# Kernel tuning notes

Measured on AMD Instinct MI355X. Metric: run time of the kernel, lower is better.

## Reference

```python
import jax, jax.numpy as jnp
import numpy as np

D_MODEL = 1024
NUM_HEADS = 16
D_K = D_MODEL // NUM_HEADS
D_FF = 4096


def setup_inputs() -> dict:
    key = jax.random.key(0)
    ks = jax.random.split(key, 12)
    s = 1.0 / np.sqrt(D_MODEL)
    sf = 1.0 / np.sqrt(D_FF)
    return {
        "x": jax.random.normal(ks[0], (2, 2048, D_MODEL), dtype=jnp.float32),
        # nn.Linear weights are [out_features, in_features]
        "Wq": jax.random.uniform(ks[1], (D_MODEL, D_MODEL), jnp.float32, -s, s),
        "Wk": jax.random.uniform(ks[2], (D_MODEL, D_MODEL), jnp.float32, -s, s),
        "Wv": jax.random.uniform(ks[3], (D_MODEL, D_MODEL), jnp.float32, -s, s),
        "Wo": jax.random.uniform(ks[4], (D_MODEL, D_MODEL), jnp.float32, -s, s),
        "W1": jax.random.uniform(ks[5], (D_FF, D_MODEL), jnp.float32, -s, s),
        "W2": jax.random.uniform(ks[6], (D_MODEL, D_FF), jnp.float32, -sf, sf),
        "g1": jnp.ones((D_MODEL,), jnp.float32),
        "b1": jnp.zeros((D_MODEL,), jnp.float32),
        "g2": jnp.ones((D_MODEL,), jnp.float32),
        "b2": jnp.zeros((D_MODEL,), jnp.float32),
    }


def _layer_norm(x, gamma, beta, eps=1e-5):
    mu = jnp.mean(x, axis=-1, keepdims=True)
    var = jnp.mean((x - mu) ** 2, axis=-1, keepdims=True)
    return (x - mu) * jax.lax.rsqrt(var + eps) * gamma + beta


def reference(x, Wq, Wk, Wv, Wo, W1, W2, g1, b1, g2, b2):
    B, S, _ = x.shape
    H, Dk = NUM_HEADS, D_K
    # projections (Linear: x @ W.T), split heads -> [B, H, S, Dk]
    q = (x @ Wq.T).reshape(B, S, H, Dk).transpose(0, 2, 1, 3)
    k = (x @ Wk.T).reshape(B, S, H, Dk).transpose(0, 2, 1, 3)
    v = (x @ Wv.T).reshape(B, S, H, Dk).transpose(0, 2, 1, 3)
    scores = jnp.einsum('bhsd,bhtd->bhst', q, k) / jnp.sqrt(jnp.float32(Dk))
    attn = jax.nn.softmax(scores, axis=-1)
    out = jnp.einsum('bhst,bhtd->bhsd', attn, v)
    out = out.transpose(0, 2, 1, 3).reshape(B, S, H * Dk)
    out = out @ Wo.T
    x_after_attn = _layer_norm(x + out, g1, b1)
    ff = jax.nn.gelu(x_after_attn @ W1.T, approximate=False)
    ff_out = ff @ W2.T
    return _layer_norm(x_after_attn + ff_out, g2, b2)
```

## Files before the change

### kernel.cpp

```cpp
#include <hip/hip_runtime.h>
#include <hip/hip_bf16.h>
#include <cstdint>
#include <cstddef>

#define D_MODEL 1024
#define D_FF    4096
#define NTOK    4096
#define SEQ     2048
#define NH      16
#define DK      64
#define LDQ     3072

typedef __bf16 bf16;
typedef __bf16 bf16_8 __attribute__((ext_vector_type(8)));
typedef __bf16 bf16_4 __attribute__((ext_vector_type(4)));
typedef float  f32_4  __attribute__((ext_vector_type(4)));

__device__ __forceinline__ void async_copy16(const bf16* g, bf16* l) {
    __builtin_amdgcn_global_load_lds((const __attribute__((address_space(1))) void*)g,
                                     (__attribute__((address_space(3))) void*)l,
                                     16, 0, 0);
}

__global__ __launch_bounds__(256)
void castk(const float* __restrict__ s, bf16* __restrict__ d, int n) {
    int i = (blockIdx.x * 256 + threadIdx.x) * 4;
    if (i < n) {
        float4 v = *(const float4*)(s + i);
        bf16_4 o;
        o[0] = (bf16)v.x; o[1] = (bf16)v.y; o[2] = (bf16)v.z; o[3] = (bf16)v.w;
        *(bf16_4*)(d + i) = o;
    }
}

template <int EPI, int BN>
__global__ __launch_bounds__(256, 2)
void gemm_bt(const bf16* __restrict__ A, const bf16* __restrict__ B,
             void* __restrict__ Cv, int M, int N, int K) {
    constexpr int NI = BN / 32;
    __shared__ bf16 As[128 * 32];
    __shared__ bf16 Bs[BN * 32];
    const int tid  = threadIdx.x;
    const int wave = tid >> 6, lane = tid & 63;
    const int quad = lane >> 4, l15 = lane & 15;
    const int wm = wave >> 1, wn = wave & 1;
    const int bm = blockIdx.x, bn = blockIdx.y;

    const bf16* A0 = A + (size_t)bm * 128 * K;
    const bf16* B0 = B + (size_t)bn * BN * K;

    f32_4 acc[4][NI];
#pragma unroll
    for (int i = 0; i < 4; i++)
#pragma unroll
        for (int j = 0; j < NI; j++) acc[i][j] = (f32_4){0.f, 0.f, 0.f, 0.f};

    const int ra = tid >> 2;
    const int ca = (tid & 3) * 8;

    for (int k0 = 0; k0 < K; k0 += 32) {
#pragma unroll
        for (int c = 0; c < 2; c++)
            async_copy16(&A0[(size_t)(c * 64 + ra) * K + k0 + ca],
                         &As[c * 2048 + wave * 512]);
#pragma unroll
        for (int c = 0; c < BN / 64; c++)
            async_copy16(&B0[(size_t)(c * 64 + ra) * K + k0 + ca],
                         &Bs[c * 2048 + wave * 512]);
        __syncthreads();

        bf16_8 af[4], bfr[NI];
#pragma unroll
        for (int mi = 0; mi < 4; mi++)
            af[mi] = *(const bf16_8*)&As[(wm * 64 + mi * 16 + l15) * 32 + quad * 8];
#pragma unroll
        for (int ni = 0; ni < NI; ni++)
            bfr[ni] = *(const bf16_8*)&Bs[(wn * (BN / 2) + ni * 16 + l15) * 32 + quad * 8];
#pragma unroll
        for (int mi = 0; mi < 4; mi++)
#pragma unroll
            for (int ni = 0; ni < NI; ni++)
                acc[mi][ni] = __builtin_amdgcn_mfma_f32_16x16x32_bf16(
                    af[mi], bfr[ni], acc[mi][ni], 0, 0, 0);
        __syncthreads();
    }

    const int row0 = bm * 128 + wm * 64 + quad * 4;
    const int col0 = bn * BN + wn * (BN / 2) + l15;
#pragma unroll
    for (int mi = 0; mi < 4; mi++) {
#pragma unroll
        for (int ni = 0; ni < NI; ni++) {
#pragma unroll
            for (int r = 0; r < 4; r++) {
                int row = row0 + mi * 16 + r;
                int col = col0 + ni * 16;
                size_t idx = (size_t)row * N + col;
                float v = acc[mi][ni][r];
                if (EPI == 0) {
                    ((bf16*)Cv)[idx] = (bf16)v;
                } else {
                    float g = 0.5f * v * (1.0f + erff(v * 0.70710678118654752f));
                    ((bf16*)Cv)[idx] = (bf16)g;
                }
            }
        }
    }
}

__global__ __launch_bounds__(256)
void transpose_v(const bf16* __restrict__ QKV, bf16* __restrict__ Vt) {
    __shared__ bf16 T[64 * 72];
    const int tb = blockIdx.x;
    const int cb = blockIdx.y;
    const int tid = threadIdx.x;
    const int r = tid >> 3, g = tid & 7;
#pragma unroll
    for (int c = 0; c < 2; ++c) {
        int row = c * 32 + r;
        bf16_8 v = *(const bf16_8*)&QKV[(size_t)(tb * 64 + row) * LDQ + 2048 + cb * 64 + g * 8];
        *(bf16_8*)&T[row * 72 + g * 8] = v;
    }
    __syncthreads();
    const int b  = (tb * 64) >> 11;
    const int s0 = (tb * 64) & 2047;
#pragma unroll
    for (int c = 0; c < 2; ++c) {
        int ch = c * 32 + r;
        bf16_8 v;
#pragma unroll
        for (int j = 0; j < 8; ++j) v[j] = T[(g * 8 + j) * 72 + ch];
        *(bf16_8*)&Vt[(size_t)(b * 1024 + cb * 64 + ch) * SEQ + s0 + g * 8] = v;
    }
}

__global__ __launch_bounds__(256)
void attn3(const bf16* __restrict__ QKV, const bf16* __restrict__ Vt,
           bf16* __restrict__ O) {
    __shared__ bf16 Ks[64 * 64];
    __shared__ bf16 Vs[64 * 64];
    __shared__ bf16 Ps[4][16 * 80];

    const int tid  = threadIdx.x;
    const int wave = tid >> 6, lane = tid & 63;
    const int quad = lane >> 4, l15 = lane & 15;
    const int qb = blockIdx.x & 31;
    const int h  = (blockIdx.x >> 5) & 15;
    const int b  = blockIdx.x >> 9;

    const bf16* Qg = QKV + (size_t)(b * SEQ) * LDQ + h * 64;
    const bf16* Kg = QKV + (size_t)(b * SEQ) * LDQ + 1024 + h * 64;
    const bf16* Vg = Vt + (size_t)(b * 1024 + h * 64) * SEQ;

    const int qrow = qb * 64 + wave * 16 + l15;
    const bf16_8 qf0 = *(const bf16_8*)&Qg[(size_t)qrow * LDQ + quad * 8];
    const bf16_8 qf1 = *(const bf16_8*)&Qg[(size_t)qrow * LDQ + 32 + quad * 8];

    const int srow = wave * 8 + (lane >> 3);
    const int sg   = lane & 7;
    const int xl   = l15 & 7;

    float l_lane = 0.f;
    f32_4 o_acc[4];
#pragma unroll
    for (int d = 0; d < 4; d++) o_acc[d] = (f32_4){0.f, 0.f, 0.f, 0.f};

    bf16* P = Ps[wave];

    for (int t = 0; t < SEQ / 64; ++t) {
        const int k0 = t * 64;
        __syncthreads();
#pragma unroll
        for (int c = 0; c < 2; ++c) {
            int r = c * 32 + srow;
            async_copy16(&Kg[(size_t)(k0 + r) * LDQ + ((sg ^ (r & 7)) * 8)],
                         &Ks[c * 2048 + wave * 512]);
            async_copy16(&Vg[(size_t)r * SEQ + k0 + ((sg ^ (r & 7)) * 8)],
                         &Vs[c * 2048 + wave * 512]);
        }
        __syncthreads();

        f32_4 s[4];
#pragma unroll
        for (int ni = 0; ni < 4; ni++) {
            const bf16* kp = &Ks[(ni * 16 + l15) * 64];
            bf16_8 kb0 = *(const bf16_8*)&kp[(quad ^ xl) * 8];
            bf16_8 kb1 = *(const bf16_8*)&kp[((quad + 4) ^ xl) * 8];
            f32_4 z = (f32_4){0.f, 0.f, 0.f, 0.f};
            s[ni] = __builtin_amdgcn_mfma_f32_16x16x32_bf16(kb0, qf0, z, 0, 0, 0);
            s[ni] = __builtin_amdgcn_mfma_f32_16x16x32_bf16(kb1, qf1, s[ni], 0, 0, 0);
        }

#pragma unroll
        for (int ni = 0; ni < 4; ni++) {
            bf16_4 pk;
#pragma unroll
            for (int r = 0; r < 4; r++) {
                float p = __expf(fmaf(s[ni][r], 0.125f, -8.0f));
                l_lane += p;
                pk[r] = (bf16)p;
            }
            int G = ni * 2 + (quad >> 1);
            *(bf16_4*)&P[l15 * 80 + ((G ^ xl) * 8) + ((quad & 1) * 4)] = pk;
        }
        bf16_8 pf0 = *(const bf16_8*)&P[l15 * 80 + ((quad ^ xl) * 8)];
        bf16_8 pf1 = *(const bf16_8*)&P[l15 * 80 + (((quad + 4) ^ xl) * 8)];

#pragma unroll
        for (int dt = 0; dt < 4; dt++) {
            const bf16* vp = &Vs[(dt * 16 + l15) * 64];
            bf16_8 vb0 = *(const bf16_8*)&vp[(quad ^ xl) * 8];
            bf16_8 vb1 = *(const bf16_8*)&vp[((quad + 4) ^ xl) * 8];
            o_acc[dt] = __builtin_amdgcn_mfma_f32_16x16x32_bf16(vb0, pf0, o_acc[dt], 0, 0, 0);
            o_acc[dt] = __builtin_amdgcn_mfma_f32_16x16x32_bf16(vb1, pf1, o_acc[dt], 0, 0, 0);
        }
    }

    l_lane += __shfl_xor(l_lane, 16);
    l_lane += __shfl_xor(l_lane, 32);
    const float rl = 1.0f / l_lane;

#pragma unroll
    for (int dt = 0; dt < 4; dt++) {
        bf16_4 pk;
#pragma unroll
        for (int r = 0; r < 4; r++) pk[r] = (bf16)(o_acc[dt][r] * rl);
        int G = dt * 2 + (quad >> 1);
        *(bf16_4*)&P[l15 * 80 + ((G ^ xl) * 8) + ((quad & 1) * 4)] = pk;
    }
    const int q2 = lane >> 2, dc = lane & 3, x2 = q2 & 7;
    bf16_8 o0 = *(const bf16_8*)&P[q2 * 80 + (((dc * 2) ^ x2) * 8)];
    bf16_8 o1 = *(const bf16_8*)&P[q2 * 80 + (((dc * 2 + 1) ^ x2) * 8)];
    const size_t row = (size_t)b * SEQ + qb * 64 + wave * 16 + q2;
    *(bf16_8*)&O[row * D_MODEL + h * 64 + dc * 16] = o0;
    *(bf16_8*)&O[row * D_MODEL + h * 64 + dc * 16 + 8] = o1;
}

template <bool A32, bool O32>
__global__ __launch_bounds__(256)
void ln_kernel(const void* __restrict__ av, const bf16* __restrict__ bb,
               const float* __restrict__ gamma, const float* __restrict__ beta,
               void* __restrict__ yv) {
    const int row = blockIdx.x;
    const int tid = threadIdx.x;
    const size_t off = (size_t)row * D_MODEL;
    float v[4];
    {
        bf16_4 xb = *(const bf16_4*)(bb + off + tid * 4);
        if (A32) {
            float4 xa = *(const float4*)((const float*)av + off + tid * 4);
            v[0] = xa.x + (float)xb[0]; v[1] = xa.y + (float)xb[1];
            v[2] = xa.z + (float)xb[2]; v[3] = xa.w + (float)xb[3];
        } else {
            bf16_4 xa = *(const bf16_4*)((const bf16*)av + off + tid * 4);
#pragma unroll
            for (int i = 0; i < 4; i++) v[i] = (float)xa[i] + (float)xb[i];
        }
    }
    float s = v[0] + v[1] + v[2] + v[3];
    float ss = v[0] * v[0] + v[1] * v[1] + v[2] * v[2] + v[3] * v[3];
#pragma unroll
    for (int m = 1; m < 64; m <<= 1) {
        s  += __shfl_xor(s, m);
        ss += __shfl_xor(ss, m);
    }
    __shared__ float red_s[4], red_q[4];
    int wave = tid >> 6, lane = tid & 63;
    if (lane == 0) { red_s[wave] = s; red_q[wave] = ss; }
    __syncthreads();
    s  = red_s[0] + red_s[1] + red_s[2] + red_s[3];
    ss = red_q[0] + red_q[1] + red_q[2] + red_q[3];
    float mu   = s * (1.f / D_MODEL);
    float var  = ss * (1.f / D_MODEL) - mu * mu;
    float rstd = rsqrtf(var + 1e-5f);
    float4 gg = *(const float4*)(gamma + tid * 4);
    float4 be = *(const float4*)(beta + tid * 4);
    float y0 = (v[0] - mu) * rstd * gg.x + be.x;
    float y1 = (v[1] - mu) * rstd * gg.y + be.y;
    float y2 = (v[2] - mu) * rstd * gg.z + be.z;
    float y3 = (v[3] - mu) * rstd * gg.w + be.w;
    if (O32) {
        *(float4*)((float*)yv + off + tid * 4) = make_float4(y0, y1, y2, y3);
    } else {
        bf16_4 o;
        o[0] = (bf16)y0; o[1] = (bf16)y1; o[2] = (bf16)y2; o[3] = (bf16)y3;
        *(bf16_4*)((bf16*)yv + off + tid * 4) = o;
    }
}

extern "C" void kernel_launch(void* const* d_in, const int* in_sizes, int n_in,
                              void* d_out, int out_size, void* d_ws, size_t ws_size,
                              hipStream_t stream) {
    (void)in_sizes; (void)n_in; (void)out_size; (void)ws_size;
    const float* x  = (const float*)d_in[0];
    const float* Wq = (const float*)d_in[1];
    const float* Wk = (const float*)d_in[2];
    const float* Wv = (const float*)d_in[3];
    const float* Wo = (const float*)d_in[4];
    const float* W1 = (const float*)d_in[5];
    const float* W2 = (const float*)d_in[6];
    const float* g1 = (const float*)d_in[7];
    const float* b1 = (const float*)d_in[8];
    const float* g2 = (const float*)d_in[9];
    const float* b2 = (const float*)d_in[10];

    char* ws = (char*)d_ws;
    bf16*  xb    = (bf16*)(ws + 0);
    bf16*  QKVb  = (bf16*)(ws + 8388608);
    bf16*  Vtb   = (bf16*)(ws + 33554432);
    bf16*  hb    = (bf16*)(ws + 8388608);
    bf16*  aob   = xb;
    bf16*  Wqkvb = (bf16*)(ws + 41943040);
    bf16*  Wob   = (bf16*)(ws + 48234496);
    bf16*  W1b   = (bf16*)(ws + 50331648);
    bf16*  W2b   = (bf16*)(ws + 58720256);
    bf16*  projb = (bf16*)(ws + 67108864);
    bf16*  ln1b  = (bf16*)(ws + 75497472);

    auto cast = [&](const float* s, bf16* d, int n) {
        castk<<<dim3((n / 4 + 255) / 256), 256, 0, stream>>>(s, d, n);
    };
    cast(x,  xb,  NTOK * D_MODEL);
    cast(Wq, Wqkvb,                   D_MODEL * D_MODEL);
    cast(Wk, Wqkvb + 1024 * 1024,     D_MODEL * D_MODEL);
    cast(Wv, Wqkvb + 2 * 1024 * 1024, D_MODEL * D_MODEL);
    cast(Wo, Wob, D_MODEL * D_MODEL);
    cast(W1, W1b, D_FF * D_MODEL);
    cast(W2, W2b, D_MODEL * D_FF);

    gemm_bt<0, 128><<<dim3(NTOK / 128, 3072 / 128), 256, 0, stream>>>(
        xb, Wqkvb, QKVb, NTOK, 3072, D_MODEL);

    transpose_v<<<dim3(NTOK / 64, D_MODEL / 64), 256, 0, stream>>>(QKVb, Vtb);

    attn3<<<dim3(1024), 256, 0, stream>>>(QKVb, Vtb, aob);

    gemm_bt<0, 64><<<dim3(NTOK / 128, D_MODEL / 64), 256, 0, stream>>>(
        aob, Wob, projb, NTOK, D_MODEL, D_MODEL);
    ln_kernel<true, false><<<NTOK, 256, 0, stream>>>(x, projb, g1, b1, ln1b);

    gemm_bt<2, 128><<<dim3(NTOK / 128, D_FF / 128), 256, 0, stream>>>(
        ln1b, W1b, hb, NTOK, D_FF, D_MODEL);
    gemm_bt<0, 64><<<dim3(NTOK / 128, D_MODEL / 64), 256, 0, stream>>>(
        hb, W2b, projb, NTOK, D_MODEL, D_FF);
    ln_kernel<false, true><<<NTOK, 256, 0, stream>>>(ln1b, projb, g2, b2, d_out);
}
```

Before: 372.4 us.

## Split-K output GEMMs, swizzle LDS reads, and merge weight casts into one launch

Folds all seven fp32-to-bf16 casts into a single kernel launch. Switches the N=1024 GEMMs from 128x64 tiles to 128x128 tiles with a split-K of 2, writing two bf16 partials that the layernorm kernels sum. Adds an XOR swizzle on the LDS tile layout to cut bank conflicts on fragment reads. The split-K keeps the grid size while raising per-tile reuse, at the cost of extra partial-output traffic and an extra bf16 rounding of partial sums.

```diff
diff --git a/kernel.cpp b/kernel.cpp
--- a/kernel.cpp
+++ b/kernel.cpp
@@ -23,74 +23,90 @@
 }
 
 __global__ __launch_bounds__(256)
-void castk(const float* __restrict__ s, bf16* __restrict__ d, int n) {
-    int i = (blockIdx.x * 256 + threadIdx.x) * 4;
-    if (i < n) {
-        float4 v = *(const float4*)(s + i);
-        bf16_4 o;
-        o[0] = (bf16)v.x; o[1] = (bf16)v.y; o[2] = (bf16)v.z; o[3] = (bf16)v.w;
-        *(bf16_4*)(d + i) = o;
-    }
-}
-
-template <int EPI, int BN>
+void cast_all(const float* __restrict__ x,  const float* __restrict__ Wq,
+              const float* __restrict__ Wk, const float* __restrict__ Wv,
+              const float* __restrict__ Wo, const float* __restrict__ W1,
+              const float* __restrict__ W2,
+              bf16* __restrict__ xb, bf16* __restrict__ Wqkvb,
+              bf16* __restrict__ Wob, bf16* __restrict__ W1b,
+              bf16* __restrict__ W2b) {
+    const int blk = blockIdx.x;
+    const float* s; bf16* d; int off;
+    if (blk < 4096)       { s = x;  d = xb;              off = blk; }
+    else if (blk < 5120)  { s = Wq; d = Wqkvb;           off = blk - 4096; }
+    else if (blk < 6144)  { s = Wk; d = Wqkvb + 1048576; off = blk - 5120; }
+    else if (blk < 7168)  { s = Wv; d = Wqkvb + 2097152; off = blk - 6144; }
+    else if (blk < 8192)  { s = Wo; d = Wob;             off = blk - 7168; }
+    else if (blk < 12288) { s = W1; d = W1b;             off = blk - 8192; }
+    else                  { s = W2; d = W2b;             off = blk - 12288; }
+    const int i = off * 1024 + threadIdx.x * 4;
+    float4 v = *(const float4*)(s + i);
+    bf16_4 o;
+    o[0] = (bf16)v.x; o[1] = (bf16)v.y; o[2] = (bf16)v.z; o[3] = (bf16)v.w;
+    *(bf16_4*)(d + i) = o;
+}
+
+template <int EPI>
 __global__ __launch_bounds__(256, 2)
 void gemm_bt(const bf16* __restrict__ A, const bf16* __restrict__ B,
-             void* __restrict__ Cv, int M, int N, int K) {
-    constexpr int NI = BN / 32;
+             bf16* __restrict__ C0, bf16* __restrict__ C1,
+             int M, int N, int ldk, int kLen) {
     __shared__ bf16 As[128 * 32];
-    __shared__ bf16 Bs[BN * 32];
+    __shared__ bf16 Bs[128 * 32];
     const int tid  = threadIdx.x;
     const int wave = tid >> 6, lane = tid & 63;
     const int quad = lane >> 4, l15 = lane & 15;
     const int wm = wave >> 1, wn = wave & 1;
-    const int bm = blockIdx.x, bn = blockIdx.y;
-
-    const bf16* A0 = A + (size_t)bm * 128 * K;
-    const bf16* B0 = B + (size_t)bn * BN * K;
-
-    f32_4 acc[4][NI];
+    const int bm = blockIdx.x, bn = blockIdx.y, z = blockIdx.z;
+
+    const bf16* A0 = A + (size_t)bm * 128 * ldk + (size_t)z * kLen;
+    const bf16* B0 = B + (size_t)bn * 128 * ldk + (size_t)z * kLen;
+
+    f32_4 acc[4][4];
 #pragma unroll
     for (int i = 0; i < 4; i++)
 #pragma unroll
-        for (int j = 0; j < NI; j++) acc[i][j] = (f32_4){0.f, 0.f, 0.f, 0.f};
+        for (int j = 0; j < 4; j++) acc[i][j] = (f32_4){0.f, 0.f, 0.f, 0.f};
 
     const int ra = tid >> 2;
-    const int ca = (tid & 3) * 8;
-
-    for (int k0 = 0; k0 < K; k0 += 32) {
+    const int gl = (tid & 3) ^ ((ra >> 1) & 3);
+    const int ca = gl * 8;
+    const int sx = (l15 >> 1) & 3;
+
+    for (int k0 = 0; k0 < kLen; k0 += 32) {
 #pragma unroll
         for (int c = 0; c < 2; c++)
-            async_copy16(&A0[(size_t)(c * 64 + ra) * K + k0 + ca],
+            async_copy16(&A0[(size_t)(c * 64 + ra) * ldk + k0 + ca],
                          &As[c * 2048 + wave * 512]);
 #pragma unroll
-        for (int c = 0; c < BN / 64; c++)
-            async_copy16(&B0[(size_t)(c * 64 + ra) * K + k0 + ca],
+        for (int c = 0; c < 2; c++)
+            async_copy16(&B0[(size_t)(c * 64 + ra) * ldk + k0 + ca],
                          &Bs[c * 2048 + wave * 512]);
         __syncthreads();
 
-        bf16_8 af[4], bfr[NI];
+        bf16_8 af[4], bfr[4];
 #pragma unroll
         for (int mi = 0; mi < 4; mi++)
-            af[mi] = *(const bf16_8*)&As[(wm * 64 + mi * 16 + l15) * 32 + quad * 8];
-#pragma unroll
-        for (int ni = 0; ni < NI; ni++)
-            bfr[ni] = *(const bf16_8*)&Bs[(wn * (BN / 2) + ni * 16 + l15) * 32 + quad * 8];
+            af[mi] = *(const bf16_8*)&As[(wm * 64 + mi * 16 + l15) * 32 + ((quad ^ sx) * 8)];
+#pragma unroll
+        for (int ni = 0; ni < 4; ni++)
+            bfr[ni] = *(const bf16_8*)&Bs[(wn * 64 + ni * 16 + l15) * 32 + ((quad ^ sx) * 8)];
 #pragma unroll
         for (int mi = 0; mi < 4; mi++)
 #pragma unroll
-            for (int ni = 0; ni < NI; ni++)
+            for (int ni = 0; ni < 4; ni++)
                 acc[mi][ni] = __builtin_amdgcn_mfma_f32_16x16x32_bf16(
                     af[mi], bfr[ni], acc[mi][ni], 0, 0, 0);
         __syncthreads();
     }
 
+    bf16* C = z ? C1 : C0;
     const int row0 = bm * 128 + wm * 64 + quad * 4;
-    const int col0 = bn * BN + wn * (BN / 2) + l15;
+    const int col0 = bn * 128 + wn * 64 + l15;
 #pragma unroll
     for (int mi = 0; mi < 4; mi++) {
 #pragma unroll
-        for (int ni = 0; ni < NI; ni++) {
+        for (int ni = 0; ni < 4; ni++) {
 #pragma unroll
             for (int r = 0; r < 4; r++) {
                 int row = row0 + mi * 16 + r;
@@ -98,10 +114,10 @@
                 size_t idx = (size_t)row * N + col;
                 float v = acc[mi][ni][r];
                 if (EPI == 0) {
-                    ((bf16*)Cv)[idx] = (bf16)v;
+                    C[idx] = (bf16)v;
                 } else {
                     float g = 0.5f * v * (1.0f + erff(v * 0.70710678118654752f));
-                    ((bf16*)Cv)[idx] = (bf16)g;
+                    C[idx] = (bf16)g;
                 }
             }
         }
@@ -238,7 +254,8 @@
 
 template <bool A32, bool O32>
 __global__ __launch_bounds__(256)
-void ln_kernel(const void* __restrict__ av, const bf16* __restrict__ bb,
+void ln_kernel(const void* __restrict__ av, const bf16* __restrict__ b0,
+               const bf16* __restrict__ b1,
                const float* __restrict__ gamma, const float* __restrict__ beta,
                void* __restrict__ yv) {
     const int row = blockIdx.x;
@@ -246,15 +263,19 @@
     const size_t off = (size_t)row * D_MODEL;
     float v[4];
     {
-        bf16_4 xb = *(const bf16_4*)(bb + off + tid * 4);
+        bf16_4 p0 = *(const bf16_4*)(b0 + off + tid * 4);
+        bf16_4 p1 = *(const bf16_4*)(b1 + off + tid * 4);
         if (A32) {
             float4 xa = *(const float4*)((const float*)av + off + tid * 4);
-            v[0] = xa.x + (float)xb[0]; v[1] = xa.y + (float)xb[1];
-            v[2] = xa.z + (float)xb[2]; v[3] = xa.w + (float)xb[3];
+            v[0] = xa.x + (float)p0[0] + (float)p1[0];
+            v[1] = xa.y + (float)p0[1] + (float)p1[1];
+            v[2] = xa.z + (float)p0[2] + (float)p1[2];
+            v[3] = xa.w + (float)p0[3] + (float)p1[3];
         } else {
             bf16_4 xa = *(const bf16_4*)((const bf16*)av + off + tid * 4);
 #pragma unroll
-            for (int i = 0; i < 4; i++) v[i] = (float)xa[i] + (float)xb[i];
+            for (int i = 0; i < 4; i++)
+                v[i] = (float)xa[i] + (float)p0[i] + (float)p1[i];
         }
     }
     float s = v[0] + v[1] + v[2] + v[3];
@@ -314,34 +335,28 @@
     bf16*  Wob   = (bf16*)(ws + 48234496);
     bf16*  W1b   = (bf16*)(ws + 50331648);
     bf16*  W2b   = (bf16*)(ws + 58720256);
-    bf16*  projb = (bf16*)(ws + 67108864);
-    bf16*  ln1b  = (bf16*)(ws + 75497472);
-
-    auto cast = [&](const float* s, bf16* d, int n) {
-        castk<<<dim3((n / 4 + 255) / 256), 256, 0, stream>>>(s, d, n);
-    };
-    cast(x,  xb,  NTOK * D_MODEL);
-    cast(Wq, Wqkvb,                   D_MODEL * D_MODEL);
-    cast(Wk, Wqkvb + 1024 * 1024,     D_MODEL * D_MODEL);
-    cast(Wv, Wqkvb + 2 * 1024 * 1024, D_MODEL * D_MODEL);
-    cast(Wo, Wob, D_MODEL * D_MODEL);
-    cast(W1, W1b, D_FF * D_MODEL);
-    cast(W2, W2b, D_MODEL * D_FF);
-
-    gemm_bt<0, 128><<<dim3(NTOK / 128, 3072 / 128), 256, 0, stream>>>(
-        xb, Wqkvb, QKVb, NTOK, 3072, D_MODEL);
+    bf16*  proj0 = (bf16*)(ws + 67108864);
+    bf16*  proj1 = (bf16*)(ws + 75497472);
+    bf16*  ln1b  = (bf16*)(ws + 83886080);
+
+    cast_all<<<dim3(16384), 256, 0, stream>>>(x, Wq, Wk, Wv, Wo, W1, W2,
+                                              xb, Wqkvb, Wob, W1b, W2b);
+
+    gemm_bt<0><<<dim3(NTOK / 128, 3072 / 128, 1), 256, 0, stream>>>(
+        xb, Wqkvb, QKVb, nullptr, NTOK, 3072, D_MODEL, D_MODEL);
 
     transpose_v<<<dim3(NTOK / 64, D_MODEL / 64), 256, 0, stream>>>(QKVb, Vtb);
 
     attn3<<<dim3(1024), 256, 0, stream>>>(QKVb, Vtb, aob);
 
-    gemm_bt<0, 64><<<dim3(NTOK / 128, D_MODEL / 64), 256, 0, stream>>>(
-        aob, Wob, projb, NTOK, D_MODEL, D_MODEL);
-    ln_kernel<true, false><<<NTOK, 256, 0, stream>>>(x, projb, g1, b1, ln1b);
-
-    gemm_bt<2, 128><<<dim3(NTOK / 128, D_FF / 128), 256, 0, stream>>>(
-        ln1b, W1b, hb, NTOK, D_FF, D_MODEL);
-    gemm_bt<0, 64><<<dim3(NTOK / 128, D_MODEL / 64), 256, 0, stream>>>(
-        hb, W2b, projb, NTOK, D_MODEL, D_FF);
-    ln_kernel<false, true><<<NTOK, 256, 0, stream>>>(ln1b, projb, g2, b2, d_out);
-}
+    gemm_bt<0><<<dim3(NTOK / 128, D_MODEL / 128, 2), 256, 0, stream>>>(
+        aob, Wob, proj0, proj1, NTOK, D_MODEL, D_MODEL, 512);
+    ln_kernel<true, false><<<NTOK, 256, 0, stream>>>(x, proj0, proj1, g1, b1, ln1b);
+
+    gemm_bt<2><<<dim3(NTOK / 128, D_FF / 128, 1), 256, 0, stream>>>(
+        ln1b, W1b, hb, nullptr, NTOK, D_FF, D_MODEL, D_MODEL);
+
+    gemm_bt<0><<<dim3(NTOK / 128, D_MODEL / 128, 2), 256, 0, stream>>>(
+        hb, W2b, proj0, proj1, NTOK, D_MODEL, D_FF, 2048);
+    ln_kernel<false, true><<<NTOK, 256, 0, stream>>>(ln1b, proj0, proj1, g2, b2, d_out);
+}
```

Result: faster. 346.5 us (-6.9%).
